# Kernel tuning notes

Hardware: AMD Instinct MI355X
Metric: run time of the kernel (lower is better)

## Reference

```python
import jax, jax.numpy as jnp
import numpy as np

DIM = 4096
N_HEADS = 32
N_KV_HEADS = 8
HEAD_DIM = DIM // N_HEADS  # 128
B, S = 2, 2048
LN_EPS = 1e-5


def _precompute_freqs_cis(seqlen, head_dim, theta=10000.0):
    inv = 1.0 / (theta ** (np.arange(0, head_dim, 2, dtype=np.float32) / head_dim))  # [HD/2]
    ang = np.outer(np.arange(seqlen, dtype=np.float32), inv)  # [S, HD/2]
    return jnp.asarray(np.stack([np.cos(ang), np.sin(ang)], axis=-1))  # [S, HD/2, 2]


def setup_inputs() -> dict:
    key = jax.random.key(0)
    ks = jax.random.split(key, 9)
    std = 0.02
    return {
        "x": jax.random.normal(ks[0], (B, S, DIM), dtype=jnp.float32),
        "freqs_cis": _precompute_freqs_cis(S, HEAD_DIM),
        "wq": jax.random.normal(ks[1], (N_HEADS * HEAD_DIM, DIM), dtype=jnp.float32) * std,
        "wk": jax.random.normal(ks[2], (N_KV_HEADS * HEAD_DIM, DIM), dtype=jnp.float32) * std,
        "wv": jax.random.normal(ks[3], (N_KV_HEADS * HEAD_DIM, DIM), dtype=jnp.float32) * std,
        "wo": jax.random.normal(ks[4], (DIM, N_HEADS * HEAD_DIM), dtype=jnp.float32) * std,
        "q_norm_w": jnp.ones((N_HEADS * HEAD_DIM,), dtype=jnp.float32),
        "q_norm_b": jnp.zeros((N_HEADS * HEAD_DIM,), dtype=jnp.float32),
        "k_norm_w": jnp.ones((N_KV_HEADS * HEAD_DIM,), dtype=jnp.float32),
        "k_norm_b": jnp.zeros((N_KV_HEADS * HEAD_DIM,), dtype=jnp.float32),
    }


def _layernorm(v, w, b):
    mu = jnp.mean(v, axis=-1, keepdims=True)
    var = jnp.var(v, axis=-1, keepdims=True)
    return (v - mu) * jax.lax.rsqrt(var + LN_EPS) * w + b


def _rope(t, fc):
    # t: [B, S, nh, HD]; fc: [S, HD/2, 2] = (cos, sin)
    b_, s_, nh, hd = t.shape
    tr = t.reshape(b_, s_, nh, hd // 2, 2)
    a, bb = tr[..., 0], tr[..., 1]
    cos = fc[None, :, None, :, 0]
    sin = fc[None, :, None, :, 1]
    out = jnp.stack([a * cos - bb * sin, a * sin + bb * cos], axis=-1)
    return out.reshape(t.shape)


def reference(x, freqs_cis, wq, wk, wv, wo, q_norm_w, q_norm_b, k_norm_w, k_norm_b):
    bsz, seqlen, _ = x.shape
    H, KV, HD = N_HEADS, N_KV_HEADS, HEAD_DIM
    R = H // KV  # GQA repeat factor

    xq = jnp.einsum('bsd,ed->bse', x, wq)
    xk = jnp.einsum('bsd,ed->bse', x, wk)
    xv = jnp.einsum('bsd,ed->bse', x, wv)

    xq = _layernorm(xq, q_norm_w, q_norm_b)
    xk = _layernorm(xk, k_norm_w, k_norm_b)

    xq = xq.reshape(bsz, seqlen, H, HD)
    xk = xk.reshape(bsz, seqlen, KV, HD)
    xv = xv.reshape(bsz, seqlen, KV, HD)

    xq = _rope(xq, freqs_cis)
    xk = _rope(xk, freqs_cis)

    # GQA: group q heads as (kv, rep) and broadcast k/v instead of materializing repeats
    xqg = xq.reshape(bsz, seqlen, KV, R, HD)
    scale = 1.0 / jnp.sqrt(jnp.float32(HD))
    scores = jnp.einsum('bqkrh,bskh->bkrqs', xqg, xk) * scale  # [B,KV,R,S,S]
    attn = jax.nn.softmax(scores, axis=-1)
    out = jnp.einsum('bkrqs,bskh->bqkrh', attn, xv).reshape(bsz, seqlen, H * HD)
    return jnp.einsum('bse,de->bsd', out, wo)
```

## Files before the change

kernel.cpp:

```cpp
#include <hip/hip_runtime.h>
#include <cstdint>

typedef _Float16 half4v __attribute__((ext_vector_type(4)));
typedef _Float16 half8v __attribute__((ext_vector_type(8)));
typedef __fp16   fp16x2 __attribute__((ext_vector_type(2)));
typedef float    f32x4v __attribute__((ext_vector_type(4)));

#define DIM    4096
#define SEQ    2048
#define NBATCH 2
#define NHEAD  32
#define NKVH   8
#define HDIM   128
#define MROWS  (NBATCH*SEQ)
#define QKV_N  6144
#define KOFF   4096
#define VOFF   5120

__device__ __forceinline__ void gl_lds16(const void* g, void* l) {
  __builtin_amdgcn_global_load_lds(
      (const __attribute__((address_space(1))) void*)g,
      (__attribute__((address_space(3))) void*)l, 16, 0, 0);
}

__global__ __launch_bounds__(256) void cvt_kernel(const float* __restrict__ in,
                                                  _Float16* __restrict__ out, int n8) {
  int stride = gridDim.x * blockDim.x;
  for (int i = blockIdx.x * blockDim.x + threadIdx.x; i < n8; i += stride) {
    const float4* p = (const float4*)(in + (size_t)i * 8);
    float4 a = p[0], b = p[1];
    half8v h;
    h[0] = (_Float16)a.x; h[1] = (_Float16)a.y; h[2] = (_Float16)a.z; h[3] = (_Float16)a.w;
    h[4] = (_Float16)b.x; h[5] = (_Float16)b.y; h[6] = (_Float16)b.z; h[7] = (_Float16)b.w;
    *(half8v*)(out + (size_t)i * 8) = h;
  }
}

#define SBAR() do { asm volatile("" ::: "memory"); \
                    __builtin_amdgcn_s_barrier();  \
                    asm volatile("" ::: "memory"); } while (0)
#define LGK0() asm volatile("s_waitcnt lgkmcnt(0)" ::: "memory")
#define VM6()  asm volatile("s_waitcnt vmcnt(6)" ::: "memory")
#define VM4()  asm volatile("s_waitcnt vmcnt(4)" ::: "memory")
#define VM0()  asm volatile("s_waitcnt vmcnt(0)" ::: "memory")

#define STAGE_HALF(Gm, rowbase, kidx, h, buf) do {                                   \
    gl_lds16((Gm) + (size_t)((rowbase) + (h)*128 + srow) * K + (kidx)*64 + sslot8,   \
             (buf) + (h)*8192 + w*512);                                              \
    gl_lds16((Gm) + (size_t)((rowbase) + (h)*128 + 64 + srow) * K + (kidx)*64 + sslot8, \
             (buf) + (h)*8192 + 4096 + w*512);                                       \
  } while (0)

#define MFMA_Q(hm, hn, bf)                                                   \
    _Pragma("unroll") for (int kk = 0; kk < 2; ++kk)                         \
      _Pragma("unroll") for (int mi = 0; mi < 4; ++mi)                       \
        _Pragma("unroll") for (int ni = 0; ni < 2; ++ni)                     \
          acc[(hm) * 4 + mi][(hn) * 2 + ni] =                                \
              __builtin_amdgcn_mfma_f32_16x16x32_f16(                        \
                  a[mi][kk], bf[ni][kk], acc[(hm) * 4 + mi][(hn) * 2 + ni], 0, 0, 0)

#define KSTEP(kcur, AC, BC, AN)                                              \
  do {                                                                       \
    const int k_ = (kcur);                                                   \
    half8v a[4][2], b0[2][2], b1[2][2];                                      \
                                         \
    _Pragma("unroll") for (int mi = 0; mi < 4; ++mi)                         \
      _Pragma("unroll") for (int kk = 0; kk < 2; ++kk)                       \
        a[mi][kk] = *(const half8v*)((AC) + (wm * 128 + mi * 16 + li) * 64 + \
                                     (((kk * 4 + g) ^ li7) * 8));            \
    _Pragma("unroll") for (int ni = 0; ni < 2; ++ni)                         \
      _Pragma("unroll") for (int kk = 0; kk < 2; ++kk)                       \
        b0[ni][kk] = *(const half8v*)((BC) + (wn * 64 + ni * 16 + li) * 64 + \
                                      (((kk * 4 + g) ^ li7) * 8));           \
    if (k_ + 1 < nkt) STAGE_HALF(A, bm, k_ + 1, 1, (AN));                    \
    SBAR(); LGK0();                                                          \
    __builtin_amdgcn_s_setprio(1);                                           \
    MFMA_Q(0, 0, b0);                                                        \
    __builtin_amdgcn_s_setprio(0);                                           \
    SBAR();                                                                  \
                                         \
    _Pragma("unroll") for (int ni = 0; ni < 2; ++ni)                         \
      _Pragma("unroll") for (int kk = 0; kk < 2; ++kk)                       \
        b1[ni][kk] = *(const half8v*)((BC) + (wn * 64 + 32 + ni * 16 + li) * 64 + \
                                      (((kk * 4 + g) ^ li7) * 8));           \
    SBAR(); LGK0();                                                          \
    __builtin_amdgcn_s_setprio(1);                                           \
    MFMA_Q(0, 1, b1);                                                        \
    __builtin_amdgcn_s_setprio(0);                                           \
    SBAR();                                                                  \
          \
    _Pragma("unroll") for (int mi = 0; mi < 4; ++mi)                         \
      _Pragma("unroll") for (int kk = 0; kk < 2; ++kk)                       \
        a[mi][kk] = *(const half8v*)((AC) + (wm * 128 + 64 + mi * 16 + li) * 64 + \
                                     (((kk * 4 + g) ^ li7) * 8));            \
    if (k_ + 2 < nkt) {                                                      \
      STAGE_HALF(B, bn, k_ + 2, 0, (BC));                                    \
      STAGE_HALF(B, bn, k_ + 2, 1, (BC));                                    \
    }                                                                        \
    SBAR(); LGK0();                                                          \
    __builtin_amdgcn_s_setprio(1);                                           \
    MFMA_Q(1, 1, b1);                                                        \
    __builtin_amdgcn_s_setprio(0);                                           \
    SBAR();                                                                  \
          \
    if (k_ + 2 < nkt) STAGE_HALF(A, bm, k_ + 2, 0, (AC));                    \
    SBAR();                                                                  \
    __builtin_amdgcn_s_setprio(1);                                           \
    MFMA_Q(1, 0, b0);                                                        \
    __builtin_amdgcn_s_setprio(0);                                           \
    if (k_ + 2 < nkt) { VM6(); } else if (k_ + 1 < nkt) { VM0(); }           \
    SBAR();                                                                  \
  } while (0)

#define HKSTEP(kcur, AC, BC, AN)                                             \
  do {                                                                       \
    const int k_ = (kcur);                                                   \
    half8v a[4][2], bb[2][2];                                                \
                                                     \
    _Pragma("unroll") for (int mi = 0; mi < 4; ++mi)                         \
      _Pragma("unroll") for (int kk = 0; kk < 2; ++kk)                       \
        a[mi][kk] = *(const half8v*)((AC) + (wm * 128 + mi * 16 + li) * 64 + \
                                     (((kk * 4 + g) ^ li7) * 8));            \
    _Pragma("unroll") for (int ni = 0; ni < 2; ++ni)                         \
      _Pragma("unroll") for (int kk = 0; kk < 2; ++kk)                       \
        bb[ni][kk] = *(const half8v*)((BC) + (wn * 32 + ni * 16 + li) * 64 + \
                                      (((kk * 4 + g) ^ li7) * 8));           \
    if (k_ + 1 < nkt) STAGE_HALF(A, bm2, k_ + 1, 1, (AN));                   \
    SBAR(); LGK0();                                                          \
    __builtin_amdgcn_s_setprio(1);                                           \
    _Pragma("unroll") for (int kk = 0; kk < 2; ++kk)                         \
      _Pragma("unroll") for (int mi = 0; mi < 4; ++mi)                       \
        _Pragma("unroll") for (int ni = 0; ni < 2; ++ni)                     \
          acc2[mi][ni] = __builtin_amdgcn_mfma_f32_16x16x32_f16(             \
              a[mi][kk], bb[ni][kk], acc2[mi][ni], 0, 0, 0);                 \
    __builtin_amdgcn_s_setprio(0);                                           \
    SBAR();                                                                  \
                            \
    _Pragma("unroll") for (int mi = 0; mi < 4; ++mi)                         \
      _Pragma("unroll") for (int kk = 0; kk < 2; ++kk)                       \
        a[mi][kk] = *(const half8v*)((AC) + (wm * 128 + 64 + mi * 16 + li) * 64 + \
                                     (((kk * 4 + g) ^ li7) * 8));            \
    if (k_ + 2 < nkt) {                                                      \
      STAGE_HALF(B, bn2, k_ + 2, 0, (BC));                                   \
      STAGE_HALF(A, bm2, k_ + 2, 0, (AC));                                   \
    }                                                                        \
    SBAR(); LGK0();                                                          \
    __builtin_amdgcn_s_setprio(1);                                           \
    _Pragma("unroll") for (int kk = 0; kk < 2; ++kk)                         \
      _Pragma("unroll") for (int mi = 0; mi < 4; ++mi)                       \
        _Pragma("unroll") for (int ni = 0; ni < 2; ++ni)                     \
          acc2[4 + mi][ni] = __builtin_amdgcn_mfma_f32_16x16x32_f16(         \
              a[mi][kk], bb[ni][kk], acc2[4 + mi][ni], 0, 0, 0);             \
    __builtin_amdgcn_s_setprio(0);                                           \
    if (k_ + 2 < nkt) { VM4(); } else if (k_ + 1 < nkt) { VM0(); }           \
    SBAR();                                                                  \
  } while (0)

template<int OUTF16>
__global__ __launch_bounds__(512, 2) void gemm256(const _Float16* __restrict__ A,
                                                  const _Float16* __restrict__ B,
                                                  void* __restrict__ Cp,
                                                  int N, int K, int nbx) {
  __shared__ __align__(16) _Float16 As[2][256 * 64];
  __shared__ __align__(16) _Float16 Bs[2][256 * 64];
  const int tid = threadIdx.x, lane = tid & 63, w = tid >> 6;
  const int g = lane >> 4, li = lane & 15, li7 = lane & 7;
  const int wm = w >> 2, wn = w & 3;
  const int nwg = gridDim.x, orig = blockIdx.x;
  const int wgid = (nwg & 7) ? orig : ((orig & 7) * (nwg >> 3) + (orig >> 3));
  const int bm = (wgid / nbx) * 256, bn = (wgid % nbx) * 256;
  const int srow = tid >> 3;
  const int sslot8 = ((lane & 7) ^ ((lane >> 3) & 7)) * 8;
  const int nkt = K >> 6;
  _Float16* As0 = &As[0][0]; _Float16* As1 = &As[1][0];
  _Float16* Bs0 = &Bs[0][0]; _Float16* Bs1 = &Bs[1][0];

  f32x4v acc[8][4] = {};

  STAGE_HALF(A, bm, 0, 0, As0);
  STAGE_HALF(A, bm, 0, 1, As0);
  STAGE_HALF(B, bn, 0, 0, Bs0);
  STAGE_HALF(B, bn, 0, 1, Bs0);
  if (nkt > 1) {
    STAGE_HALF(B, bn, 1, 0, Bs1);
    STAGE_HALF(B, bn, 1, 1, Bs1);
    STAGE_HALF(A, bm, 1, 0, As1);
    VM6();
  } else {
    VM0();
  }
  SBAR();

  for (int k = 0; k < nkt; k += 2) {
    KSTEP(k,     As0, Bs0, As1);
    KSTEP(k + 1, As1, Bs1, As0);
  }

  const int r0 = bm + wm * 128 + g * 4;
  const int c0 = bn + wn * 64 + li;
#pragma unroll
  for (int mi = 0; mi < 8; ++mi)
#pragma unroll
    for (int ni = 0; ni < 4; ++ni)
#pragma unroll
      for (int j = 0; j < 4; ++j) {
        size_t idx = (size_t)(r0 + mi * 16 + j) * N + (c0 + ni * 16);
        if (OUTF16) ((_Float16*)Cp)[idx] = (_Float16)acc[mi][ni][j];
        else        ((float*)Cp)[idx]    = acc[mi][ni][j];
      }
}

__global__ __launch_bounds__(512, 2) void gemm_qkv(const _Float16* __restrict__ A,
                                                   const _Float16* __restrict__ B,
                                                   _Float16* __restrict__ Cp) {
  __shared__ __align__(16) _Float16 As[2][256 * 64];
  __shared__ __align__(16) _Float16 Bs[2][256 * 64];
  const int tid = threadIdx.x, lane = tid & 63, w = tid >> 6;
  const int g = lane >> 4, li = lane & 15, li7 = lane & 7;
  const int wm = w >> 2, wn = w & 3;
  const int K = DIM, N = QKV_N, nkt = DIM >> 6;
  const int orig = blockIdx.x;
  const int wgid = (orig & 7) * 32 + (orig >> 3);
  const int bm = (wgid >> 4) * 256, bn = (wgid & 15) * 256;
  const int t2 = wgid >> 1;
  const int bm2 = (t2 >> 3) * 256;
  const int bn2 = (16 + (t2 & 7)) * 256 + (wgid & 1) * 128;
  const int srow = tid >> 3;
  const int sslot8 = ((lane & 7) ^ ((lane >> 3) & 7)) * 8;
  _Float16* As0 = &As[0][0]; _Float16* As1 = &As[1][0];
  _Float16* Bs0 = &Bs[0][0]; _Float16* Bs1 = &Bs[1][0];

  {
    f32x4v acc[8][4] = {};
    STAGE_HALF(A, bm, 0, 0, As0);
    STAGE_HALF(A, bm, 0, 1, As0);
    STAGE_HALF(B, bn, 0, 0, Bs0);
    STAGE_HALF(B, bn, 0, 1, Bs0);
    STAGE_HALF(B, bn, 1, 0, Bs1);
    STAGE_HALF(B, bn, 1, 1, Bs1);
    STAGE_HALF(A, bm, 1, 0, As1);
    VM6();
    SBAR();
    for (int k = 0; k < nkt; k += 2) {
      KSTEP(k,     As0, Bs0, As1);
      KSTEP(k + 1, As1, Bs1, As0);
    }
    const int r0 = bm + wm * 128 + g * 4;
    const int c0 = bn + wn * 64 + li;
#pragma unroll
    for (int mi = 0; mi < 8; ++mi)
#pragma unroll
      for (int ni = 0; ni < 4; ++ni)
#pragma unroll
        for (int j = 0; j < 4; ++j)
          Cp[(size_t)(r0 + mi * 16 + j) * N + (c0 + ni * 16)] = (_Float16)acc[mi][ni][j];
  }

  {
    f32x4v acc2[8][2] = {};
    STAGE_HALF(A, bm2, 0, 0, As0);
    STAGE_HALF(A, bm2, 0, 1, As0);
    STAGE_HALF(B, bn2, 0, 0, Bs0);
    STAGE_HALF(B, bn2, 1, 0, Bs1);
    STAGE_HALF(A, bm2, 1, 0, As1);
    VM4();
    SBAR();
    for (int k = 0; k < nkt; k += 2) {
      HKSTEP(k,     As0, Bs0, As1);
      HKSTEP(k + 1, As1, Bs1, As0);
    }
    const int r0 = bm2 + wm * 128 + g * 4;
    const int c0 = bn2 + wn * 32 + li;
#pragma unroll
    for (int mi = 0; mi < 8; ++mi)
#pragma unroll
      for (int ni = 0; ni < 2; ++ni)
#pragma unroll
        for (int j = 0; j < 4; ++j)
          Cp[(size_t)(r0 + mi * 16 + j) * N + (c0 + ni * 16)] = (_Float16)acc2[mi][ni][j];
  }
}

template<int E>
__global__ __launch_bounds__(256) void ln_rope(_Float16* __restrict__ t, int ldt,
                                               const float* __restrict__ gw,
                                               const float* __restrict__ gb,
                                               const float* __restrict__ fc) {
  constexpr int EPT = E / 256;
  const int row = blockIdx.x;
  const int s = row & (SEQ - 1);
  const int tid = threadIdx.x, lane = tid & 63, w = tid >> 6;
  _Float16* rp = t + (size_t)row * ldt + tid * EPT;
  float v[EPT];
#pragma unroll
  for (int i = 0; i < EPT; i += 4) {
    half4v hv = *(const half4v*)(rp + i);
    v[i] = (float)hv[0]; v[i+1] = (float)hv[1]; v[i+2] = (float)hv[2]; v[i+3] = (float)hv[3];
  }
  float sum = 0.f, ssq = 0.f;
#pragma unroll
  for (int i = 0; i < EPT; ++i) { sum += v[i]; ssq += v[i] * v[i]; }
#pragma unroll
  for (int off = 1; off < 64; off <<= 1) { sum += __shfl_xor(sum, off); ssq += __shfl_xor(ssq, off); }
  __shared__ float red[8];
  if (lane == 0) { red[w] = sum; red[4 + w] = ssq; }
  __syncthreads();
  sum = red[0] + red[1] + red[2] + red[3];
  ssq = red[4] + red[5] + red[6] + red[7];
  const float mu = sum * (1.0f / E);
  const float rstd = rsqrtf(ssq * (1.0f / E) - mu * mu + 1e-5f);
  float ov[EPT];
#pragma unroll
  for (int i = 0; i < EPT; i += 2) {
    int e = tid * EPT + i;
    int hd = e & (HDIM - 1);
    float2 cs = *(const float2*)(fc + (size_t)s * HDIM + (hd >> 1) * 2);
    float a = (v[i]   - mu) * rstd * gw[e]   + gb[e];
    float b = (v[i+1] - mu) * rstd * gw[e+1] + gb[e+1];
    ov[i]   = a * cs.x - b * cs.y;
    ov[i+1] = a * cs.y + b * cs.x;
  }
#pragma unroll
  for (int i = 0; i < EPT; i += 4) {
    half4v hv;
    hv[0] = (_Float16)ov[i];   hv[1] = (_Float16)ov[i+1];
    hv[2] = (_Float16)ov[i+2]; hv[3] = (_Float16)ov[i+3];
    *(half4v*)(rp + i) = hv;
  }
}

__global__ __launch_bounds__(256) void vtrans(const _Float16* __restrict__ qkv,
                                              _Float16* __restrict__ vt) {
  __shared__ _Float16 tile[64][136];
  const int blk = blockIdx.x;
  const int st = blk & 31, kvh = (blk >> 5) & 7, b = blk >> 8;
  const int t = threadIdx.x;
  const _Float16* src = qkv + (size_t)(b * SEQ + st * 64) * QKV_N + VOFF + kvh * 128;
#pragma unroll
  for (int i = 0; i < 4; ++i) {
    int sl = (t >> 4) + i * 16;
    int h0 = (t & 15) * 8;
    *(half8v*)&tile[sl][h0] = *(const half8v*)(src + (size_t)sl * QKV_N + h0);
  }
  __syncthreads();
  const int hd = t & 127, half = t >> 7;
  _Float16* dst = vt + ((size_t)((b * NKVH + kvh) * 128 + hd)) * SEQ + st * 64 + half * 32;
#pragma unroll
  for (int j = 0; j < 32; j += 8) {
    half8v v;
#pragma unroll
    for (int e = 0; e < 8; ++e) v[e] = tile[half * 32 + j + e][hd];
    *(half8v*)(dst + j) = v;
  }
}

__global__ __launch_bounds__(256, 2) void attn_kernel(const _Float16* __restrict__ QKV,
                                                      const _Float16* __restrict__ VT,
                                                      _Float16* __restrict__ Oa) {
  __shared__ __align__(16) _Float16 Ksh[2][64 * 128];
  __shared__ __align__(16) char Vsh[128 * 128];
  const int tid = threadIdx.x, lane = tid & 63, w = tid >> 6;
  const int g = lane >> 4, li = lane & 15;
  const int blk = blockIdx.x;
  const int qt = blk & 15, h = (blk >> 4) & 31, b = blk >> 9;
  const int kvh = h >> 2;
  const size_t LD = QKV_N;
  const _Float16* Qb = QKV + (size_t)(b * SEQ) * LD + h * HDIM;
  const _Float16* Kb = QKV + (size_t)(b * SEQ) * LD + KOFF + kvh * HDIM;
  const _Float16* VTb = VT + (size_t)((b * NKVH + kvh) * 128) * SEQ;
  const int lg = lane >> 4;
  const int gbit = (lane >> 5) & 1;

  half8v qf[2][4];
#pragma unroll
  for (int s = 0; s < 2; ++s) {
    const int qrow = qt * 128 + w * 32 + s * 16 + li;
#pragma unroll
    for (int kk = 0; kk < 4; ++kk) {
      half8v q0 = *(const half8v*)(Qb + (size_t)qrow * LD + kk * 32 + g * 8);
#pragma unroll
      for (int e = 0; e < 8; ++e) q0[e] = q0[e] * (_Float16)0.08838834764831845f;
      qf[s][kk] = q0;
    }
  }
  float mrow[2] = {-1e30f, -1e30f}, lrow[2] = {0.f, 0.f};
  f32x4v oacc[2][8] = {};

#define ASTAGE_K(kt_, buf_) do {                                              \
    _Pragma("unroll") for (int i_ = 0; i_ < 4; ++i_) {                        \
      int chunk = i_ * 4 + w;                                                 \
      int r = chunk * 4 + lg;                                                 \
      int sc8 = ((lane & 15) ^ (r & 7)) * 8;                                  \
      gl_lds16(Kb + (size_t)((kt_) * 64 + r) * LD + sc8, (buf_) + chunk * 512); \
    } } while (0)

#define ASTAGE_V(kt_, buf_) do {                                              \
    _Pragma("unroll") for (int i_ = 0; i_ < 4; ++i_) {                        \
      int chunk = i_ * 4 + w;                                                 \
      int hd_ = chunk * 8 + (lane >> 3);                                      \
      int keyh = (chunk ^ (lane >> 3)) & 7;                                   \
      int p_ = lane & 7;                                                      \
      gl_lds16(VTb + (size_t)hd_ * SEQ + (kt_) * 64 + ((p_ ^ keyh) * 8),      \
               (buf_) + chunk * 1024);                                        \
    } } while (0)

  ASTAGE_K(0, Ksh[0]);
  ASTAGE_V(0, Vsh);
  VM0();
  SBAR();

  const int NT = SEQ / 64;
  for (int kt = 0; kt < NT; ++kt) {
    const int cur = kt & 1;
    const _Float16* Kcur = Ksh[cur];
    f32x4v sc0[4] = {}, sc1[4] = {};
    __builtin_amdgcn_s_setprio(1);
#pragma unroll
    for (int kk = 0; kk < 4; ++kk) {
#pragma unroll
      for (int ni = 0; ni < 4; ++ni) {
        half8v kf = *(const half8v*)(Kcur + (16 * ni + li) * 128 + ((4 * kk + g) ^ (li & 7)) * 8);
        sc0[ni] = __builtin_amdgcn_mfma_f32_16x16x32_f16(kf, qf[0][kk], sc0[ni], 0, 0, 0);
        sc1[ni] = __builtin_amdgcn_mfma_f32_16x16x32_f16(kf, qf[1][kk], sc1[ni], 0, 0, 0);
      }
    }
    __builtin_amdgcn_s_setprio(0);
    if (kt + 1 < NT) ASTAGE_K(kt + 1, Ksh[cur ^ 1]);
    uint32_t u[2][4][2];
#pragma unroll
    for (int s = 0; s < 2; ++s) {
      f32x4v* sc = s ? sc1 : sc0;
      float m16 = sc[0][0];
#pragma unroll
      for (int ni = 0; ni < 4; ++ni)
        m16 = fmaxf(m16, fmaxf(fmaxf(sc[ni][0], sc[ni][1]), fmaxf(sc[ni][2], sc[ni][3])));
      m16 = fmaxf(m16, __shfl_xor(m16, 16));
      m16 = fmaxf(m16, __shfl_xor(m16, 32));
      if (!__all(m16 - mrow[s] <= 8.0f)) {
        const float mn = fmaxf(mrow[s], m16);
        const float sfo = __expf(mrow[s] - mn);
        mrow[s] = mn;
        lrow[s] *= sfo;
        float sfj[4];
#pragma unroll
        for (int j = 0; j < 4; ++j) sfj[j] = __shfl(sfo, (lane & 48) | (4 * g + j));
#pragma unroll
        for (int nio = 0; nio < 8; ++nio) {
          oacc[s][nio][0] *= sfj[0]; oacc[s][nio][1] *= sfj[1];
          oacc[s][nio][2] *= sfj[2]; oacc[s][nio][3] *= sfj[3];
        }
      }
      float rs = 0.f;
#pragma unroll
      for (int ni = 0; ni < 4; ++ni)
#pragma unroll
        for (int j = 0; j < 4; ++j) { float pv = __expf(sc[ni][j] - mrow[s]); sc[ni][j] = pv; rs += pv; }
      rs += __shfl_xor(rs, 16); rs += __shfl_xor(rs, 32);
      lrow[s] += rs;
#pragma unroll
      for (int ni = 0; ni < 4; ++ni) {
        fp16x2 p0 = __builtin_amdgcn_cvt_pkrtz(sc[ni][0], sc[ni][1]);
        fp16x2 p1 = __builtin_amdgcn_cvt_pkrtz(sc[ni][2], sc[ni][3]);
        u[s][ni][0] = *(uint32_t*)&p0;
        u[s][ni][1] = *(uint32_t*)&p1;
      }
    }
    if (kt + 1 < NT) { VM4(); } else { VM0(); }
    SBAR();
#pragma unroll
    for (int kk = 0; kk < 2; ++kk) {
      half8v pa[2];
#pragma unroll
      for (int s = 0; s < 2; ++s) {
        uint32_t own0 = gbit ? u[s][2*kk+1][0] : u[s][2*kk][0];
        uint32_t own1 = gbit ? u[s][2*kk+1][1] : u[s][2*kk][1];
        uint32_t oth0 = gbit ? u[s][2*kk][0]   : u[s][2*kk+1][0];
        uint32_t oth1 = gbit ? u[s][2*kk][1]   : u[s][2*kk+1][1];
        uint32_t r16_0 = (uint32_t)__shfl_xor((int)own0, 16);
        uint32_t r16_1 = (uint32_t)__shfl_xor((int)own1, 16);
        uint32_t r32_0 = (uint32_t)__shfl_xor((int)oth0, 32);
        uint32_t r32_1 = (uint32_t)__shfl_xor((int)oth1, 32);
        uint32_t r48_0 = (uint32_t)__shfl_xor((int)oth0, 48);
        uint32_t r48_1 = (uint32_t)__shfl_xor((int)oth1, 48);
        uint32_t d0 = (g == 0) ? own0 : (g == 1) ? r48_0 : (g == 2) ? r32_0 : r16_0;
        uint32_t d1 = (g == 0) ? own1 : (g == 1) ? r48_1 : (g == 2) ? r32_1 : r16_1;
        uint32_t d2 = (g == 0) ? r16_0 : (g == 1) ? r32_0 : (g == 2) ? r48_0 : own0;
        uint32_t d3 = (g == 0) ? r16_1 : (g == 1) ? r32_1 : (g == 2) ? r48_1 : own1;
        union { uint32_t u4[4]; half8v hh; } pu;
        pu.u4[0] = d0; pu.u4[1] = d1; pu.u4[2] = d2; pu.u4[3] = d3;
        pa[s] = pu.hh;
      }
      __builtin_amdgcn_s_setprio(1);
#pragma unroll
      for (int nio = 0; nio < 8; ++nio) {
        int r = nio * 16 + li;
        int key = ((r >> 3) ^ r) & 7;
        half8v bv = *(const half8v*)(Vsh + r * 128 + (((kk * 4 + g) ^ key) << 4));
        oacc[0][nio] = __builtin_amdgcn_mfma_f32_16x16x32_f16(pa[0], bv, oacc[0][nio], 0, 0, 0);
        oacc[1][nio] = __builtin_amdgcn_mfma_f32_16x16x32_f16(pa[1], bv, oacc[1][nio], 0, 0, 0);
      }
      __builtin_amdgcn_s_setprio(0);
    }
    VM0();
    SBAR();
    if (kt + 1 < NT) ASTAGE_V(kt + 1, Vsh);
  }
#undef ASTAGE_K
#undef ASTAGE_V
#pragma unroll
  for (int s = 0; s < 2; ++s) {
    float rinv[4];
#pragma unroll
    for (int j = 0; j < 4; ++j)
      rinv[j] = 1.0f / __shfl(lrow[s], (lane & 48) | (4 * g + j));
    _Float16* Ob = Oa + (size_t)(b * SEQ + qt * 128 + w * 32 + s * 16) * DIM + h * HDIM;
#pragma unroll
    for (int j = 0; j < 4; ++j)
#pragma unroll
      for (int nio = 0; nio < 8; ++nio)
        Ob[(size_t)(4 * g + j) * DIM + nio * 16 + li] = (_Float16)(oacc[s][nio][j] * rinv[j]);
  }
}

extern "C" void kernel_launch(void* const* d_in, const int* in_sizes, int n_in,
                              void* d_out, int out_size, void* d_ws, size_t ws_size,
                              hipStream_t stream) {
  const float* x   = (const float*)d_in[0];
  const float* fc  = (const float*)d_in[1];
  const float* wq  = (const float*)d_in[2];
  const float* wk  = (const float*)d_in[3];
  const float* wv  = (const float*)d_in[4];
  const float* wo  = (const float*)d_in[5];
  const float* qnw = (const float*)d_in[6];
  const float* qnb = (const float*)d_in[7];
  const float* knw = (const float*)d_in[8];
  const float* knb = (const float*)d_in[9];
  float* out = (float*)d_out;
  (void)in_sizes; (void)n_in; (void)out_size;

  const size_t MB = 1024 * 1024;
  if (ws_size < 128 * MB) return;
  char* ws = (char*)d_ws;
  _Float16* x_h    = (_Float16*)(ws + 0);
  _Float16* wqkv_h = (_Float16*)(ws + 32 * MB);
  _Float16* wk_h   = (_Float16*)(ws + 64 * MB);
  _Float16* wv_h   = (_Float16*)(ws + 72 * MB);
  _Float16* qkv_h  = (_Float16*)(ws + 80 * MB);
  _Float16* wo_h   = wqkv_h;
  _Float16* vt_h   = wk_h;
  _Float16* ao_h   = x_h;

  cvt_kernel<<<2048, 256, 0, stream>>>(x,  x_h,    (MROWS * DIM) / 8);
  cvt_kernel<<<2048, 256, 0, stream>>>(wq, wqkv_h, (DIM * DIM) / 8);
  cvt_kernel<<<1024, 256, 0, stream>>>(wk, wk_h,   (1024 * DIM) / 8);
  cvt_kernel<<<1024, 256, 0, stream>>>(wv, wv_h,   (1024 * DIM) / 8);

  gemm_qkv<<<256, 512, 0, stream>>>(x_h, wqkv_h, qkv_h);

  cvt_kernel<<<2048, 256, 0, stream>>>(wo, wo_h, (DIM * DIM) / 8);

  vtrans<<<NBATCH * NKVH * (SEQ / 64), 256, 0, stream>>>(qkv_h, vt_h);

  ln_rope<4096><<<MROWS, 256, 0, stream>>>(qkv_h,        QKV_N, qnw, qnb, fc);
  ln_rope<1024><<<MROWS, 256, 0, stream>>>(qkv_h + KOFF, QKV_N, knw, knb, fc);

  attn_kernel<<<NBATCH * NHEAD * (SEQ / 128), 256, 0, stream>>>(qkv_h, vt_h, ao_h);

  gemm256<0><<<(MROWS / 256) * (DIM / 256), 512, 0, stream>>>(ao_h, wo_h, out,
                                                              DIM, DIM, DIM / 256);
}
```

Baseline: 618.0 us.

## Fold softmax scale and log2e into Q during LN/RoPE, single-buffer K tile

Applies the 1/sqrt(d)·log2(e) factor to Q inside the layernorm+RoPE kernel, so the attention kernel can drop its per-element Q scaling and use exp2f instead of __expf. The lazy-rescale threshold is adjusted to base-2 units. K shared memory goes from double to single buffering: the next K tile is now issued after the barrier, during the PV phase, instead of overlapping with the softmax. This halves K LDS usage, which may allow more resident blocks, but the QK^T of the next iteration now waits on a load that previously had more time to land.

```diff
diff --git a/kernel.cpp b/kernel.cpp
--- a/kernel.cpp
+++ b/kernel.cpp
@@ -285,7 +285,8 @@
 __global__ __launch_bounds__(256) void ln_rope(_Float16* __restrict__ t, int ldt,
                                                const float* __restrict__ gw,
                                                const float* __restrict__ gb,
-                                               const float* __restrict__ fc) {
+                                               const float* __restrict__ fc,
+                                               float qs) {
   constexpr int EPT = E / 256;
   const int row = blockIdx.x;
   const int s = row & (SEQ - 1);
@@ -317,8 +318,8 @@
     float2 cs = *(const float2*)(fc + (size_t)s * HDIM + (hd >> 1) * 2);
     float a = (v[i]   - mu) * rstd * gw[e]   + gb[e];
     float b = (v[i+1] - mu) * rstd * gw[e+1] + gb[e+1];
-    ov[i]   = a * cs.x - b * cs.y;
-    ov[i+1] = a * cs.y + b * cs.x;
+    ov[i]   = (a * cs.x - b * cs.y) * qs;
+    ov[i+1] = (a * cs.y + b * cs.x) * qs;
   }
 #pragma unroll
   for (int i = 0; i < EPT; i += 4) {
@@ -357,7 +358,7 @@
 __global__ __launch_bounds__(256, 2) void attn_kernel(const _Float16* __restrict__ QKV,
                                                       const _Float16* __restrict__ VT,
                                                       _Float16* __restrict__ Oa) {
-  __shared__ __align__(16) _Float16 Ksh[2][64 * 128];
+  __shared__ __align__(16) _Float16 Ksh[64 * 128];
   __shared__ __align__(16) char Vsh[128 * 128];
   const int tid = threadIdx.x, lane = tid & 63, w = tid >> 6;
   const int g = lane >> 4, li = lane & 15;
@@ -370,18 +371,15 @@
   const _Float16* VTb = VT + (size_t)((b * NKVH + kvh) * 128) * SEQ;
   const int lg = lane >> 4;
   const int gbit = (lane >> 5) & 1;
+  const float THR = 11.541560327111707f;
 
   half8v qf[2][4];
 #pragma unroll
   for (int s = 0; s < 2; ++s) {
     const int qrow = qt * 128 + w * 32 + s * 16 + li;
 #pragma unroll
-    for (int kk = 0; kk < 4; ++kk) {
-      half8v q0 = *(const half8v*)(Qb + (size_t)qrow * LD + kk * 32 + g * 8);
-#pragma unroll
-      for (int e = 0; e < 8; ++e) q0[e] = q0[e] * (_Float16)0.08838834764831845f;
-      qf[s][kk] = q0;
-    }
+    for (int kk = 0; kk < 4; ++kk)
+      qf[s][kk] = *(const half8v*)(Qb + (size_t)qrow * LD + kk * 32 + g * 8);
   }
   float mrow[2] = {-1e30f, -1e30f}, lrow[2] = {0.f, 0.f};
   f32x4v oacc[2][8] = {};
@@ -404,28 +402,25 @@
                (buf_) + chunk * 1024);                                        \
     } } while (0)
 
-  ASTAGE_K(0, Ksh[0]);
+  ASTAGE_K(0, Ksh);
   ASTAGE_V(0, Vsh);
   VM0();
   SBAR();
 
   const int NT = SEQ / 64;
   for (int kt = 0; kt < NT; ++kt) {
-    const int cur = kt & 1;
-    const _Float16* Kcur = Ksh[cur];
     f32x4v sc0[4] = {}, sc1[4] = {};
     __builtin_amdgcn_s_setprio(1);
 #pragma unroll
     for (int kk = 0; kk < 4; ++kk) {
 #pragma unroll
       for (int ni = 0; ni < 4; ++ni) {
-        half8v kf = *(const half8v*)(Kcur + (16 * ni + li) * 128 + ((4 * kk + g) ^ (li & 7)) * 8);
+        half8v kf = *(const half8v*)(Ksh + (16 * ni + li) * 128 + ((4 * kk + g) ^ (li & 7)) * 8);
         sc0[ni] = __builtin_amdgcn_mfma_f32_16x16x32_f16(kf, qf[0][kk], sc0[ni], 0, 0, 0);
         sc1[ni] = __builtin_amdgcn_mfma_f32_16x16x32_f16(kf, qf[1][kk], sc1[ni], 0, 0, 0);
       }
     }
     __builtin_amdgcn_s_setprio(0);
-    if (kt + 1 < NT) ASTAGE_K(kt + 1, Ksh[cur ^ 1]);
     uint32_t u[2][4][2];
 #pragma unroll
     for (int s = 0; s < 2; ++s) {
@@ -436,9 +431,9 @@
         m16 = fmaxf(m16, fmaxf(fmaxf(sc[ni][0], sc[ni][1]), fmaxf(sc[ni][2], sc[ni][3])));
       m16 = fmaxf(m16, __shfl_xor(m16, 16));
       m16 = fmaxf(m16, __shfl_xor(m16, 32));
-      if (!__all(m16 - mrow[s] <= 8.0f)) {
+      if (!__all(m16 - mrow[s] <= THR)) {
         const float mn = fmaxf(mrow[s], m16);
-        const float sfo = __expf(mrow[s] - mn);
+        const float sfo = exp2f(mrow[s] - mn);
         mrow[s] = mn;
         lrow[s] *= sfo;
         float sfj[4];
@@ -454,7 +449,7 @@
 #pragma unroll
       for (int ni = 0; ni < 4; ++ni)
 #pragma unroll
-        for (int j = 0; j < 4; ++j) { float pv = __expf(sc[ni][j] - mrow[s]); sc[ni][j] = pv; rs += pv; }
+        for (int j = 0; j < 4; ++j) { float pv = exp2f(sc[ni][j] - mrow[s]); sc[ni][j] = pv; rs += pv; }
       rs += __shfl_xor(rs, 16); rs += __shfl_xor(rs, 32);
       lrow[s] += rs;
 #pragma unroll
@@ -465,8 +460,9 @@
         u[s][ni][1] = *(uint32_t*)&p1;
       }
     }
-    if (kt + 1 < NT) { VM4(); } else { VM0(); }
+    VM0();
     SBAR();
+    if (kt + 1 < NT) ASTAGE_K(kt + 1, Ksh);
 #pragma unroll
     for (int kk = 0; kk < 2; ++kk) {
       half8v pa[2];
@@ -561,8 +557,9 @@
 
   vtrans<<<NBATCH * NKVH * (SEQ / 64), 256, 0, stream>>>(qkv_h, vt_h);
 
-  ln_rope<4096><<<MROWS, 256, 0, stream>>>(qkv_h,        QKV_N, qnw, qnb, fc);
-  ln_rope<1024><<<MROWS, 256, 0, stream>>>(qkv_h + KOFF, QKV_N, knw, knb, fc);
+  const float qscale = (float)(0.08838834764831845 * 1.4426950408889634);
+  ln_rope<4096><<<MROWS, 256, 0, stream>>>(qkv_h,        QKV_N, qnw, qnb, fc, qscale);
+  ln_rope<1024><<<MROWS, 256, 0, stream>>>(qkv_h + KOFF, QKV_N, knw, knb, fc, 1.0f);
 
   attn_kernel<<<NBATCH * NHEAD * (SEQ / 128), 256, 0, stream>>>(qkv_h, vt_h, ao_h);
 
```

Result: slower. 643.6 us (+4.1%).
